# Optimization experiments

Hardware: AMD Instinct MI355X
Metric: run time of the kernel (lower is better)

## Reference

```python
import jax, jax.numpy as jnp
import numpy as np

B, T, N, F_IN = 8, 288, 2000, 1
E, ID, H, K = 128, 16, 128, 20
FL = T // 2 + 1  # rfft length = in_len//2 + 1
EPS_NORM = 1e-12
EPS_LN = 1e-8


def setup_inputs() -> dict:
    key = jax.random.key(0)
    k0, k1, k2, k3, k4 = jax.random.split(key, 5)
    return {
        "x": jax.random.normal(k0, (B, T, N, F_IN), jnp.float32),
        "Ex": jax.random.normal(k1, (FL, E), jnp.float32),
        "nodes": jax.random.normal(k2, (N, ID), jnp.float32),
        "Wd": jax.random.normal(k3, (N, E + ID, H), jnp.float32),
        "Wxabs": jax.random.normal(k4, (H, H), jnp.float32),
    }


def reference(x, Ex, nodes, Wd, Wxabs):
    # [B,T,N,F] -> take feature 0 -> [B,N,T]
    xt = jnp.transpose(x[:, :, :, 0], (0, 2, 1))
    xf = jnp.abs(jnp.fft.rfft(xt, axis=-1))  # [B,N,FL]
    # F.normalize p=2 over dim=1 (nodes), then dim=2 (freq): x / max(||x||, eps)
    xf = xf / jnp.clip(jnp.sqrt(jnp.sum(xf * xf, axis=1, keepdims=True)), EPS_NORM)
    xf = xf / jnp.clip(jnp.sqrt(jnp.sum(xf * xf, axis=2, keepdims=True)), EPS_NORM)
    xe = jnp.matmul(xf, Ex)  # [B,N,E]
    # cat(): append static node identity embedding per batch element
    xk = jnp.concatenate(
        [xe, jnp.broadcast_to(nodes, (xe.shape[0], N, ID))], axis=-1
    )  # [B,N,E+ID]
    # per-node weight bmm: [N,B,E+ID] @ [N,E+ID,H] -> [B,N,H]
    x1 = jax.nn.relu(jnp.einsum('bnd,ndh->bnh', xk, Wd))
    # LayerNorm over last two dims [N,H], eps=1e-8, no affine
    mu = jnp.mean(x1, axis=(1, 2), keepdims=True)
    var = jnp.mean((x1 - mu) ** 2, axis=(1, 2), keepdims=True)
    x2 = (x1 - mu) / jnp.sqrt(var + EPS_LN)
    # dropout is identity at inference
    adp = jnp.einsum('bnh,hk->bnk', x2, Wxabs)  # convt
    adj = jnp.einsum('bnh,bmh->bnm', adp, x1)  # [B,N,N]
    adp = jax.nn.relu(adj)
    # dy_mask_graph: per-row topk over dim=2 (torch dim=1 of the [N,N] slice),
    # binary mask via scatter of ones, then elementwise mask
    _, idx = jax.lax.top_k(adp, K)  # [B,N,K]
    bi = jnp.arange(adp.shape[0])[:, None, None]
    ni = jnp.arange(N)[None, :, None]
    mask = jnp.zeros_like(adp).at[bi, ni, idx].set(1.0)
    adj_masked = adp * mask
    return jax.nn.softmax(adj_masked, axis=2)
```

## Files before the change

kernel.cpp:

```cpp
#include <hip/hip_runtime.h>
#include <math.h>

#define BB 8
#define TT 288
#define NN 2000
#define FLEN 145
#define EE 128
#define IDD 16
#define HH 128
#define DKK 144
#define KTOP 20

#define OFF_TW  ((size_t)0)
#define SZ_TW   ((size_t)TT*FLEN*2)
#define OFF_XF  (OFF_TW + SZ_TW)
#define SZ_XF   ((size_t)BB*FLEN*NN)
#define OFF_ICN (OFF_XF + SZ_XF)
#define OFF_IRN (OFF_ICN + (size_t)BB*FLEN)
#define OFF_XE  (OFF_IRN + (size_t)BB*NN)
#define SZ_BNH  ((size_t)BB*NN*HH)
#define OFF_X1  (OFF_XE + SZ_BNH)
#define OFF_ADP (OFF_X1 + SZ_BNH)
#define OFF_CSW (OFF_ADP + SZ_BNH)
#define OFF_LNS (OFF_CSW + HH)
#define OFF_LNF (OFF_LNS + 16)

__device__ __forceinline__ float wredSum(float v) {
#pragma unroll
  for (int o = 32; o > 0; o >>= 1) v += __shfl_down(v, o, 64);
  return v;
}
__device__ __forceinline__ float wredMax(float v) {
#pragma unroll
  for (int o = 32; o > 0; o >>= 1) v = fmaxf(v, __shfl_down(v, o, 64));
  return v;
}

__global__ void k_init(const float* __restrict__ Wx, float* __restrict__ csw,
                       float* __restrict__ lns) {
  int k = threadIdx.x;
  float s = 0.f;
  for (int h = 0; h < HH; ++h) s += Wx[h * HH + k];
  csw[k] = s;
  if (k < 16) lns[k] = 0.f;
}

__global__ void k_tw(float* __restrict__ tw) {
  int id = blockIdx.x * 256 + threadIdx.x;
  if (id >= TT * FLEN) return;
  int t = id / FLEN, f = id % FLEN;
  int r = (t * f) % TT;
  double th = -2.0 * 3.14159265358979323846 * (double)r / (double)TT;
  tw[2 * id]     = (float)cos(th);
  tw[2 * id + 1] = (float)sin(th);
}

__global__ void k_dft(const float* __restrict__ x, const float* __restrict__ tw,
                      float* __restrict__ xf) {
  __shared__ __align__(16) float Xs[16][128];
  __shared__ __align__(16) float TWs[16][32][2];
  const int b = blockIdx.z;
  const int f0 = blockIdx.y * 32;
  const int n0 = blockIdx.x * 128;
  const int tid = threadIdx.x;
  const int tn = tid & 31;
  const int tf = tid >> 5;
  float ar[4][4] = {}, ai[4][4] = {};
  for (int t0 = 0; t0 < TT; t0 += 16) {
    __syncthreads();
    for (int l = tid; l < 512; l += 256) {
      int row = l >> 5, q = l & 31;
      int n = n0 + q * 4;
      const float* src = x + ((size_t)b * TT + (t0 + row)) * NN + n;
      float4 v = make_float4(0, 0, 0, 0);
      if (n + 3 < NN) v = *(const float4*)src;
      else {
        if (n + 0 < NN) v.x = src[0];
        if (n + 1 < NN) v.y = src[1];
        if (n + 2 < NN) v.z = src[2];
        if (n + 3 < NN) v.w = src[3];
      }
      *(float4*)&Xs[row][q * 4] = v;
    }
    for (int l = tid; l < 512; l += 256) {
      int row = l >> 5, ff = l & 31;
      int f = f0 + ff;
      float2 cs = make_float2(0, 0);
      if (f < FLEN) cs = *(const float2*)&tw[((size_t)(t0 + row) * FLEN + f) * 2];
      *(float2*)&TWs[row][ff][0] = cs;
    }
    __syncthreads();
#pragma unroll 4
    for (int t = 0; t < 16; ++t) {
      float4 xv = *(float4*)&Xs[t][tn * 4];
      float xx[4] = {xv.x, xv.y, xv.z, xv.w};
      float4 p0 = *(float4*)&TWs[t][tf * 4][0];
      float4 p1 = *(float4*)&TWs[t][tf * 4 + 2][0];
      float c[4] = {p0.x, p0.z, p1.x, p1.z};
      float s[4] = {p0.y, p0.w, p1.y, p1.w};
#pragma unroll
      for (int i = 0; i < 4; ++i)
#pragma unroll
        for (int j = 0; j < 4; ++j) {
          ar[i][j] = fmaf(xx[j], c[i], ar[i][j]);
          ai[i][j] = fmaf(xx[j], s[i], ai[i][j]);
        }
    }
  }
#pragma unroll
  for (int i = 0; i < 4; ++i) {
    int f = f0 + tf * 4 + i;
    if (f >= FLEN) continue;
    float* dst = &xf[((size_t)b * FLEN + f) * NN];
    float o[4];
#pragma unroll
    for (int j = 0; j < 4; ++j)
      o[j] = sqrtf(ar[i][j] * ar[i][j] + ai[i][j] * ai[i][j]);
    int n = n0 + tn * 4;
    if (n + 3 < NN) *(float4*)&dst[n] = make_float4(o[0], o[1], o[2], o[3]);
    else {
#pragma unroll
      for (int j = 0; j < 4; ++j) if (n + j < NN) dst[n + j] = o[j];
    }
  }
}

__global__ void k_colnorm(const float* __restrict__ xf, float* __restrict__ icn) {
  __shared__ float sc[4];
  int bf = blockIdx.x;
  const float* rowp = xf + (size_t)bf * NN;
  float s = 0.f;
  for (int i = threadIdx.x; i < NN; i += 256) { float v = rowp[i]; s = fmaf(v, v, s); }
  s = wredSum(s);
  int lane = threadIdx.x & 63, w = threadIdx.x >> 6;
  if (lane == 0) sc[w] = s;
  __syncthreads();
  if (threadIdx.x == 0)
    icn[bf] = 1.f / fmaxf(sqrtf(sc[0] + sc[1] + sc[2] + sc[3]), 1e-12f);
}

__global__ void k_rownorm(const float* __restrict__ xf, const float* __restrict__ icn,
                          float* __restrict__ irn) {
  int b = blockIdx.y;
  int n = blockIdx.x * 256 + threadIdx.x;
  if (n >= NN) return;
  float s = 0.f;
  for (int f = 0; f < FLEN; ++f) {
    float v = xf[((size_t)b * FLEN + f) * NN + n] * icn[b * FLEN + f];
    s = fmaf(v, v, s);
  }
  irn[b * NN + n] = 1.f / fmaxf(sqrtf(s), 1e-12f);
}

__global__ void k_xe(const float* __restrict__ xf, const float* __restrict__ icn,
                     const float* __restrict__ irn, const float* __restrict__ Ex,
                     float* __restrict__ xe) {
  __shared__ __align__(16) float As[16][64];
  __shared__ __align__(16) float Bs[16][128];
  const int b = blockIdx.y;
  const int n0 = blockIdx.x * 64;
  const int tid = threadIdx.x;
  const int tn = tid >> 4, te = tid & 15;
  float acc[4][8] = {};
  for (int f0 = 0; f0 < 160; f0 += 16) {
    __syncthreads();
    {
      int kt = tid >> 4, q = tid & 15;
      int f = f0 + kt;
      int n = n0 + q * 4;
      float4 v = make_float4(0, 0, 0, 0);
      if (f < FLEN) {
        float ic = icn[b * FLEN + f];
        const float* src = &xf[((size_t)b * FLEN + f) * NN + n];
        if (n + 3 < NN) v = *(const float4*)src;
        else {
          if (n + 0 < NN) v.x = src[0];
          if (n + 1 < NN) v.y = src[1];
          if (n + 2 < NN) v.z = src[2];
          if (n + 3 < NN) v.w = src[3];
        }
        v.x *= ic; v.y *= ic; v.z *= ic; v.w *= ic;
      }
      *(float4*)&As[kt][q * 4] = v;
    }
    for (int l = tid; l < 512; l += 256) {
      int kt = l >> 5, q = l & 31;
      int f = f0 + kt;
      float4 v = make_float4(0, 0, 0, 0);
      if (f < FLEN) v = *(const float4*)&Ex[(size_t)f * EE + q * 4];
      *(float4*)&Bs[kt][q * 4] = v;
    }
    __syncthreads();
#pragma unroll
    for (int k = 0; k < 16; ++k) {
      float4 a  = *(float4*)&As[k][tn * 4];
      float4 b0 = *(float4*)&Bs[k][te * 4];
      float4 b1 = *(float4*)&Bs[k][64 + te * 4];
      float av[4] = {a.x, a.y, a.z, a.w};
      float bv[8] = {b0.x, b0.y, b0.z, b0.w, b1.x, b1.y, b1.z, b1.w};
#pragma unroll
      for (int i = 0; i < 4; ++i)
#pragma unroll
        for (int j = 0; j < 8; ++j)
          acc[i][j] = fmaf(av[i], bv[j], acc[i][j]);
    }
  }
#pragma unroll
  for (int i = 0; i < 4; ++i) {
    int n = n0 + tn * 4 + i;
    if (n >= NN) continue;
    float sc = irn[b * NN + n];
    float* dst = &xe[((size_t)b * NN + n) * EE];
    *(float4*)&dst[te * 4] =
        make_float4(acc[i][0] * sc, acc[i][1] * sc, acc[i][2] * sc, acc[i][3] * sc);
    *(float4*)&dst[64 + te * 4] =
        make_float4(acc[i][4] * sc, acc[i][5] * sc, acc[i][6] * sc, acc[i][7] * sc);
  }
}

__global__ void k_x1(const float* __restrict__ xe, const float* __restrict__ nodes,
                     const float* __restrict__ Wd, float* __restrict__ x1) {
  __shared__ __align__(16) float xk[8][DKK];
  const int n = blockIdx.x;
  const int tid = threadIdx.x;
  {
    int b = tid >> 5, q = tid & 31;
    *(float4*)&xk[b][q * 4] = *(const float4*)&xe[((size_t)b * NN + n) * EE + q * 4];
  }
  if (tid < 128) {
    int b = tid >> 4, i = tid & 15;
    xk[b][EE + i] = nodes[(size_t)n * IDD + i];
  }
  __syncthreads();
  const int h = tid & 127;
  const int bg = tid >> 7;
  float acc[4] = {0.f, 0.f, 0.f, 0.f};
  const float* w = Wd + (size_t)n * DKK * HH + h;
  for (int d = 0; d < DKK; ++d) {
    float wv = w[(size_t)d * HH];
#pragma unroll
    for (int j = 0; j < 4; ++j) acc[j] = fmaf(xk[bg + 2 * j][d], wv, acc[j]);
  }
#pragma unroll
  for (int j = 0; j < 4; ++j) {
    int b = bg + 2 * j;
    x1[((size_t)b * NN + n) * HH + h] = fmaxf(acc[j], 0.f);
  }
}

__global__ void k_ln_stats(const float* __restrict__ x1, float* __restrict__ lns) {
  __shared__ float sc[4], sc2[4];
  int b = blockIdx.y, chunk = blockIdx.x;
  const float* base = x1 + (size_t)b * NN * HH + (size_t)chunk * 8000;
  float s = 0.f, s2 = 0.f;
  for (int i = threadIdx.x; i < 8000; i += 256) {
    float v = base[i];
    s += v; s2 = fmaf(v, v, s2);
  }
  s = wredSum(s); s2 = wredSum(s2);
  int lane = threadIdx.x & 63, w = threadIdx.x >> 6;
  if (lane == 0) { sc[w] = s; sc2[w] = s2; }
  __syncthreads();
  if (threadIdx.x == 0) {
    atomicAdd(&lns[b], sc[0] + sc[1] + sc[2] + sc[3]);
    atomicAdd(&lns[8 + b], sc2[0] + sc2[1] + sc2[2] + sc2[3]);
  }
}

__global__ void k_ln_final(const float* __restrict__ lns, float* __restrict__ lnf) {
  int b = threadIdx.x;
  if (b < 8) {
    float cnt = (float)(NN * HH);
    float mu = lns[b] / cnt;
    float var = fmaxf(lns[8 + b] / cnt - mu * mu, 0.f);
    lnf[b] = mu;
    lnf[8 + b] = 1.f / sqrtf(var + 1e-8f);
  }
}

__global__ void k_adp(const float* __restrict__ x1, const float* __restrict__ Wx,
                      const float* __restrict__ csw, const float* __restrict__ lnf,
                      float* __restrict__ adp) {
  __shared__ __align__(16) float As[16][64];
  __shared__ __align__(16) float Bs[16][128];
  const int r0 = blockIdx.x * 64;
  const int tid = threadIdx.x;
  const int tn = tid >> 4, te = tid & 15;
  float acc[4][8] = {};
  for (int k0 = 0; k0 < HH; k0 += 16) {
    __syncthreads();
    {
      int rr = tid >> 2, kq = tid & 3;
      float4 v = *(const float4*)&x1[(size_t)(r0 + rr) * HH + k0 + kq * 4];
      As[kq * 4 + 0][rr] = v.x;
      As[kq * 4 + 1][rr] = v.y;
      As[kq * 4 + 2][rr] = v.z;
      As[kq * 4 + 3][rr] = v.w;
    }
    for (int l = tid; l < 512; l += 256) {
      int kt = l >> 5, q = l & 31;
      *(float4*)&Bs[kt][q * 4] = *(const float4*)&Wx[(size_t)(k0 + kt) * HH + q * 4];
    }
    __syncthreads();
#pragma unroll
    for (int k = 0; k < 16; ++k) {
      float4 a  = *(float4*)&As[k][tn * 4];
      float4 b0 = *(float4*)&Bs[k][te * 4];
      float4 b1 = *(float4*)&Bs[k][64 + te * 4];
      float av[4] = {a.x, a.y, a.z, a.w};
      float bv[8] = {b0.x, b0.y, b0.z, b0.w, b1.x, b1.y, b1.z, b1.w};
#pragma unroll
      for (int i = 0; i < 4; ++i)
#pragma unroll
        for (int j = 0; j < 8; ++j)
          acc[i][j] = fmaf(av[i], bv[j], acc[i][j]);
    }
  }
  float4 c0 = *(const float4*)&csw[te * 4];
  float4 c1 = *(const float4*)&csw[64 + te * 4];
  float cw[8] = {c0.x, c0.y, c0.z, c0.w, c1.x, c1.y, c1.z, c1.w};
#pragma unroll
  for (int i = 0; i < 4; ++i) {
    int r = r0 + tn * 4 + i;
    int b = r / NN;
    float mu = lnf[b], isd = lnf[8 + b];
    float* dst = &adp[(size_t)r * HH];
    float o[8];
#pragma unroll
    for (int j = 0; j < 8; ++j) o[j] = (acc[i][j] - mu * cw[j]) * isd;
    *(float4*)&dst[te * 4] = make_float4(o[0], o[1], o[2], o[3]);
    *(float4*)&dst[64 + te * 4] = make_float4(o[4], o[5], o[6], o[7]);
  }
}

__global__ void k_adj(const float* __restrict__ adp, const float* __restrict__ x1,
                      float* __restrict__ out) {
  __shared__ __align__(16) float As[32][128];
  __shared__ __align__(16) float Bs[32][128];
  const int b = blockIdx.z;
  const int n0 = blockIdx.y * 128;
  const int m0 = blockIdx.x * 128;
  const int tid = threadIdx.x;
  const int tn = tid >> 4, tm = tid & 15;
  float acc[8][8] = {};
  for (int k0 = 0; k0 < HH; k0 += 32) {
    __syncthreads();
    for (int l = tid; l < 1024; l += 256) {
      int row = l >> 3, kq = l & 7;
      int n = n0 + row;
      float4 v = make_float4(0, 0, 0, 0);
      if (n < NN) v = *(const float4*)&adp[((size_t)b * NN + n) * HH + k0 + kq * 4];
      As[kq * 4 + 0][row] = v.x; As[kq * 4 + 1][row] = v.y;
      As[kq * 4 + 2][row] = v.z; As[kq * 4 + 3][row] = v.w;
    }
    for (int l = tid; l < 1024; l += 256) {
      int row = l >> 3, kq = l & 7;
      int m = m0 + row;
      float4 v = make_float4(0, 0, 0, 0);
      if (m < NN) v = *(const float4*)&x1[((size_t)b * NN + m) * HH + k0 + kq * 4];
      Bs[kq * 4 + 0][row] = v.x; Bs[kq * 4 + 1][row] = v.y;
      Bs[kq * 4 + 2][row] = v.z; Bs[kq * 4 + 3][row] = v.w;
    }
    __syncthreads();
#pragma unroll 4
    for (int k = 0; k < 32; ++k) {
      float4 a0 = *(float4*)&As[k][tn * 4];
      float4 a1 = *(float4*)&As[k][64 + tn * 4];
      float4 bq0 = *(float4*)&Bs[k][tm * 4];
      float4 bq1 = *(float4*)&Bs[k][64 + tm * 4];
      float av[8] = {a0.x, a0.y, a0.z, a0.w, a1.x, a1.y, a1.z, a1.w};
      float bv[8] = {bq0.x, bq0.y, bq0.z, bq0.w, bq1.x, bq1.y, bq1.z, bq1.w};
#pragma unroll
      for (int i = 0; i < 8; ++i)
#pragma unroll
        for (int j = 0; j < 8; ++j)
          acc[i][j] = fmaf(av[i], bv[j], acc[i][j]);
    }
  }
  const bool mfull = (m0 + 128 <= NN);
#pragma unroll
  for (int ih = 0; ih < 2; ++ih) {
#pragma unroll
    for (int i = 0; i < 4; ++i) {
      int n = n0 + ih * 64 + tn * 4 + i;
      if (n >= NN) continue;
      float* dst = &out[((size_t)b * NN + n) * NN + m0];
      float r[8];
#pragma unroll
      for (int j = 0; j < 8; ++j) r[j] = fmaxf(acc[ih * 4 + i][j], 0.f);
      if (mfull) {
        *(float4*)&dst[tm * 4] = make_float4(r[0], r[1], r[2], r[3]);
        *(float4*)&dst[64 + tm * 4] = make_float4(r[4], r[5], r[6], r[7]);
      } else {
#pragma unroll
        for (int j = 0; j < 4; ++j) { int m = tm * 4 + j; if (m0 + m < NN) dst[m] = r[j]; }
#pragma unroll
        for (int j = 0; j < 4; ++j) { int m = 64 + tm * 4 + j; if (m0 + m < NN) dst[m] = r[4 + j]; }
      }
    }
  }
}

__global__ void k_softmax(float* __restrict__ out) {
  __shared__ __align__(16) float row[NN];
  __shared__ float scr[4];
  __shared__ float swv[4];
  __shared__ int swi[4];
  __shared__ float tkv[KTOP];
  __shared__ int tki[KTOP];
  __shared__ float bcast[1];
  const int r = blockIdx.x;
  float* g = out + (size_t)r * NN;
  const int tid = threadIdx.x;
  const int lane = tid & 63, w = tid >> 6;
  for (int q = tid; q < 500; q += 256) *(float4*)&row[q * 4] = *(const float4*)&g[q * 4];
  __syncthreads();
  float m = 0.f;
  for (int i = tid; i < NN; i += 256) m = fmaxf(m, row[i]);
  m = wredMax(m);
  if (lane == 0) scr[w] = m;
  __syncthreads();
  m = fmaxf(fmaxf(scr[0], scr[1]), fmaxf(scr[2], scr[3]));
  const float thr = m - 87.f;
  float s = 0.f, c = 0.f;
  for (int i = tid; i < NN; i += 256) {
    float v = row[i];
    if (v > thr) { s += expf(v - m); c += 1.f; }
  }
  s = wredSum(s); c = wredSum(c);
  __syncthreads();
  if (lane == 0) scr[w] = s;
  __syncthreads();
  s = scr[0] + scr[1] + scr[2] + scr[3];
  __syncthreads();
  if (lane == 0) scr[w] = c;
  __syncthreads();
  c = scr[0] + scr[1] + scr[2] + scr[3];
  const float em = expf(-m);
  if (c <= 20.5f) {
    float D = s + ((float)NN - c) * em;
    float invD = 1.f / D;
    float defv = em * invD;
    for (int q = tid; q < 500; q += 256) {
      float4 v = *(float4*)&row[q * 4];
      float4 o;
      o.x = (v.x > thr) ? expf(v.x - m) * invD : defv;
      o.y = (v.y > thr) ? expf(v.y - m) * invD : defv;
      o.z = (v.z > thr) ? expf(v.z - m) * invD : defv;
      o.w = (v.w > thr) ? expf(v.w - m) * invD : defv;
      *(float4*)&g[q * 4] = o;
    }
  } else {
    for (int it = 0; it < KTOP; ++it) {
      float bv = -1.f; int bi = 0x7fffffff;
      for (int i = tid; i < NN; i += 256) {
        float v = row[i];
        if (v > bv) { bv = v; bi = i; }
      }
#pragma unroll
      for (int o = 32; o > 0; o >>= 1) {
        float ov = __shfl_down(bv, o, 64);
        int oi = __shfl_down(bi, o, 64);
        if (ov > bv || (ov == bv && oi < bi)) { bv = ov; bi = oi; }
      }
      __syncthreads();
      if (lane == 0) { swv[w] = bv; swi[w] = bi; }
      __syncthreads();
      if (tid == 0) {
        float fv = swv[0]; int fi = swi[0];
        for (int ww = 1; ww < 4; ++ww)
          if (swv[ww] > fv || (swv[ww] == fv && swi[ww] < fi)) { fv = swv[ww]; fi = swi[ww]; }
        tkv[it] = fv; tki[it] = fi;
        row[fi] = -1.f;
      }
      __syncthreads();
    }
    if (tid == 0) {
      float D = ((float)(NN - KTOP)) * em;
      for (int it = 0; it < KTOP; ++it) D += expf(tkv[it] - m);
      bcast[0] = 1.f / D;
    }
    __syncthreads();
    float invD = bcast[0];
    float defv = em * invD;
    for (int q = tid; q < 500; q += 256)
      *(float4*)&g[q * 4] = make_float4(defv, defv, defv, defv);
    __syncthreads();
    if (tid < KTOP) g[tki[tid]] = expf(tkv[tid] - m) * invD;
  }
}

extern "C" void kernel_launch(void* const* d_in, const int* in_sizes, int n_in,
                              void* d_out, int out_size, void* d_ws, size_t ws_size,
                              hipStream_t stream) {
  const float* x     = (const float*)d_in[0];
  const float* Ex    = (const float*)d_in[1];
  const float* nodes = (const float*)d_in[2];
  const float* Wd    = (const float*)d_in[3];
  const float* Wx    = (const float*)d_in[4];
  float* out = (float*)d_out;
  float* w = (float*)d_ws;
  float* tw  = w + OFF_TW;
  float* xf  = w + OFF_XF;
  float* icn = w + OFF_ICN;
  float* irn = w + OFF_IRN;
  float* xe  = w + OFF_XE;
  float* x1  = w + OFF_X1;
  float* adp = w + OFF_ADP;
  float* csw = w + OFF_CSW;
  float* lns = w + OFF_LNS;
  float* lnf = w + OFF_LNF;

  k_init<<<1, 128, 0, stream>>>(Wx, csw, lns);
  k_tw<<<(TT * FLEN + 255) / 256, 256, 0, stream>>>(tw);
  k_dft<<<dim3(16, 5, BB), 256, 0, stream>>>(x, tw, xf);
  k_colnorm<<<BB * FLEN, 256, 0, stream>>>(xf, icn);
  k_rownorm<<<dim3(8, BB), 256, 0, stream>>>(xf, icn, irn);
  k_xe<<<dim3(32, BB), 256, 0, stream>>>(xf, icn, irn, Ex, xe);
  k_x1<<<NN, 256, 0, stream>>>(xe, nodes, Wd, x1);
  k_ln_stats<<<dim3(32, BB), 256, 0, stream>>>(x1, lns);
  k_ln_final<<<1, 64, 0, stream>>>(lns, lnf);
  k_adp<<<250, 256, 0, stream>>>(x1, Wx, csw, lnf, adp);
  k_adj<<<dim3(16, 16, BB), 256, 0, stream>>>(adp, x1, out);
  k_softmax<<<BB * NN, 256, 0, stream>>>(out);
}
```

Before: 541.0 us.

## Use split-fp16 MFMA for adjacency GEMM and restructure per-node x1 matmul

```diff
diff --git a/kernel.cpp b/kernel.cpp
--- a/kernel.cpp
+++ b/kernel.cpp
@@ -10,6 +10,10 @@
 #define HH 128
 #define DKK 144
 #define KTOP 20
+
+typedef _Float16 half8 __attribute__((ext_vector_type(8)));
+typedef float f32x4 __attribute__((ext_vector_type(4)));
+typedef unsigned short ushort_t;
 
 #define OFF_TW  ((size_t)0)
 #define SZ_TW   ((size_t)TT*FLEN*2)
@@ -34,6 +38,14 @@
 #pragma unroll
   for (int o = 32; o > 0; o >>= 1) v = fmaxf(v, __shfl_down(v, o, 64));
   return v;
+}
+
+__device__ __forceinline__ void split16(float v, ushort_t& hi, ushort_t& lo) {
+  _Float16 h = (_Float16)v;
+  _Float16 l = (_Float16)(v - (float)h);
+  union { _Float16 f; ushort_t u; } a, b;
+  a.f = h; b.f = l;
+  hi = a.u; lo = b.u;
 }
 
 __global__ void k_init(const float* __restrict__ Wx, float* __restrict__ csw,
@@ -218,9 +230,11 @@
   }
 }
 
-__global__ void k_x1(const float* __restrict__ xe, const float* __restrict__ nodes,
-                     const float* __restrict__ Wd, float* __restrict__ x1) {
+__global__ void k_x1(const float* xe, const float* __restrict__ nodes,
+                     const float* __restrict__ Wd, float* __restrict__ x1,
+                     ushort_t* x1hl) {
   __shared__ __align__(16) float xk[8][DKK];
+  __shared__ float red[4][32][33];
   const int n = blockIdx.x;
   const int tid = threadIdx.x;
   {
@@ -232,19 +246,47 @@
     xk[b][EE + i] = nodes[(size_t)n * IDD + i];
   }
   __syncthreads();
-  const int h = tid & 127;
-  const int bg = tid >> 7;
-  float acc[4] = {0.f, 0.f, 0.f, 0.f};
-  const float* w = Wd + (size_t)n * DKK * HH + h;
-  for (int d = 0; d < DKK; ++d) {
-    float wv = w[(size_t)d * HH];
-#pragma unroll
-    for (int j = 0; j < 4; ++j) acc[j] = fmaf(xk[bg + 2 * j][d], wv, acc[j]);
-  }
-#pragma unroll
-  for (int j = 0; j < 4; ++j) {
-    int b = bg + 2 * j;
-    x1[((size_t)b * NN + n) * HH + h] = fmaxf(acc[j], 0.f);
+  const int h4 = tid & 31;
+  const int dg = tid >> 5;
+  float acc[8][4] = {};
+  for (int d = dg; d < DKK; d += 8) {
+    float4 wv = *(const float4*)&Wd[((size_t)n * DKK + d) * HH + h4 * 4];
+#pragma unroll
+    for (int b = 0; b < 8; ++b) {
+      float xv = xk[b][d];
+      acc[b][0] = fmaf(xv, wv.x, acc[b][0]);
+      acc[b][1] = fmaf(xv, wv.y, acc[b][1]);
+      acc[b][2] = fmaf(xv, wv.z, acc[b][2]);
+      acc[b][3] = fmaf(xv, wv.w, acc[b][3]);
+    }
+  }
+#pragma unroll
+  for (int b = 0; b < 8; ++b)
+#pragma unroll
+    for (int j = 0; j < 4; ++j)
+      acc[b][j] += __shfl_xor(acc[b][j], 32, 64);
+  const int wv_ = tid >> 6, lane = tid & 63;
+  if (lane < 32) {
+#pragma unroll
+    for (int b = 0; b < 8; ++b)
+#pragma unroll
+      for (int j = 0; j < 4; ++j)
+        red[wv_][lane][b * 4 + j] = acc[b][j];
+  }
+  __syncthreads();
+#pragma unroll
+  for (int o = 0; o < 4; ++o) {
+    int idx = tid + o * 256;
+    int b = idx >> 7, h = idx & 127;
+    float s = red[0][h >> 2][b * 4 + (h & 3)] + red[1][h >> 2][b * 4 + (h & 3)] +
+              red[2][h >> 2][b * 4 + (h & 3)] + red[3][h >> 2][b * 4 + (h & 3)];
+    s = fmaxf(s, 0.f);
+    x1[((size_t)b * NN + n) * HH + h] = s;
+    ushort_t hi, lo;
+    split16(s, hi, lo);
+    size_t base = ((size_t)b * NN + n) * 256;
+    x1hl[base + h] = hi;
+    x1hl[base + 128 + h] = lo;
   }
 }
 
@@ -280,7 +322,7 @@
 
 __global__ void k_adp(const float* __restrict__ x1, const float* __restrict__ Wx,
                       const float* __restrict__ csw, const float* __restrict__ lnf,
-                      float* __restrict__ adp) {
+                      ushort_t* __restrict__ adphl) {
   __shared__ __align__(16) float As[16][64];
   __shared__ __align__(16) float Bs[16][128];
   const int r0 = blockIdx.x * 64;
@@ -324,78 +366,97 @@
     int r = r0 + tn * 4 + i;
     int b = r / NN;
     float mu = lnf[b], isd = lnf[8 + b];
-    float* dst = &adp[(size_t)r * HH];
-    float o[8];
-#pragma unroll
-    for (int j = 0; j < 8; ++j) o[j] = (acc[i][j] - mu * cw[j]) * isd;
-    *(float4*)&dst[te * 4] = make_float4(o[0], o[1], o[2], o[3]);
-    *(float4*)&dst[64 + te * 4] = make_float4(o[4], o[5], o[6], o[7]);
-  }
-}
-
-__global__ void k_adj(const float* __restrict__ adp, const float* __restrict__ x1,
+    size_t base = (size_t)r * 256;
+    ushort_t hi[8], lo[8];
+#pragma unroll
+    for (int j = 0; j < 8; ++j) {
+      float o = (acc[i][j] - mu * cw[j]) * isd;
+      split16(o, hi[j], lo[j]);
+    }
+    ushort4 u;
+    u.x = hi[0]; u.y = hi[1]; u.z = hi[2]; u.w = hi[3];
+    *(ushort4*)&adphl[base + te * 4] = u;
+    u.x = hi[4]; u.y = hi[5]; u.z = hi[6]; u.w = hi[7];
+    *(ushort4*)&adphl[base + 64 + te * 4] = u;
+    u.x = lo[0]; u.y = lo[1]; u.z = lo[2]; u.w = lo[3];
+    *(ushort4*)&adphl[base + 128 + te * 4] = u;
+    u.x = lo[4]; u.y = lo[5]; u.z = lo[6]; u.w = lo[7];
+    *(ushort4*)&adphl[base + 128 + 64 + te * 4] = u;
+  }
+}
+
+__global__ void k_adj(const ushort_t* __restrict__ adphl,
+                      const ushort_t* __restrict__ x1hl,
                       float* __restrict__ out) {
-  __shared__ __align__(16) float As[32][128];
-  __shared__ __align__(16) float Bs[32][128];
+  __shared__ __align__(16) ushort_t lds[4][128 * 32];
   const int b = blockIdx.z;
   const int n0 = blockIdx.y * 128;
   const int m0 = blockIdx.x * 128;
   const int tid = threadIdx.x;
-  const int tn = tid >> 4, tm = tid & 15;
-  float acc[8][8] = {};
+  const int w = tid >> 6;
+  const int lane = tid & 63;
+  const int quad = lane >> 4, r16 = lane & 15;
+  const int rBase = (w >> 1) * 64;
+  const int cBase = (w & 1) * 64;
+
+  f32x4 acc[4][4];
+#pragma unroll
+  for (int i = 0; i < 4; ++i)
+#pragma unroll
+    for (int j = 0; j < 4; ++j)
+      acc[i][j] = (f32x4){0.f, 0.f, 0.f, 0.f};
+
+  const ushort_t* src = (w < 2) ? adphl : x1hl;
+  const int rg0 = (w < 2) ? n0 : m0;
+  const int loOff = (w & 1) ? 128 : 0;
+
   for (int k0 = 0; k0 < HH; k0 += 32) {
     __syncthreads();
-    for (int l = tid; l < 1024; l += 256) {
-      int row = l >> 3, kq = l & 7;
-      int n = n0 + row;
-      float4 v = make_float4(0, 0, 0, 0);
-      if (n < NN) v = *(const float4*)&adp[((size_t)b * NN + n) * HH + k0 + kq * 4];
-      As[kq * 4 + 0][row] = v.x; As[kq * 4 + 1][row] = v.y;
-      As[kq * 4 + 2][row] = v.z; As[kq * 4 + 3][row] = v.w;
-    }
-    for (int l = tid; l < 1024; l += 256) {
-      int row = l >> 3, kq = l & 7;
-      int m = m0 + row;
-      float4 v = make_float4(0, 0, 0, 0);
-      if (m < NN) v = *(const float4*)&x1[((size_t)b * NN + m) * HH + k0 + kq * 4];
-      Bs[kq * 4 + 0][row] = v.x; Bs[kq * 4 + 1][row] = v.y;
-      Bs[kq * 4 + 2][row] = v.z; Bs[kq * 4 + 3][row] = v.w;
-    }
-    __syncthreads();
-#pragma unroll 4
-    for (int k = 0; k < 32; ++k) {
-      float4 a0 = *(float4*)&As[k][tn * 4];
-      float4 a1 = *(float4*)&As[k][64 + tn * 4];
-      float4 bq0 = *(float4*)&Bs[k][tm * 4];
-      float4 bq1 = *(float4*)&Bs[k][64 + tm * 4];
-      float av[8] = {a0.x, a0.y, a0.z, a0.w, a1.x, a1.y, a1.z, a1.w};
-      float bv[8] = {bq0.x, bq0.y, bq0.z, bq0.w, bq1.x, bq1.y, bq1.z, bq1.w};
-#pragma unroll
-      for (int i = 0; i < 8; ++i)
-#pragma unroll
-        for (int j = 0; j < 8; ++j)
-          acc[i][j] = fmaf(av[i], bv[j], acc[i][j]);
-    }
-  }
-  const bool mfull = (m0 + 128 <= NN);
-#pragma unroll
-  for (int ih = 0; ih < 2; ++ih) {
+#pragma unroll
+    for (int i = 0; i < 8; ++i) {
+      int cl = i * 64 + lane;
+      int row = cl >> 2, c = cl & 3;
+      int gr = rg0 + row; if (gr > NN - 1) gr = NN - 1;
+      const uint4* gp =
+          (const uint4*)(src + ((size_t)(b * NN + gr)) * 256 + loOff + k0 + c * 8);
+      uint4 v = *gp;
+      *(uint4*)&lds[w][row * 32 + ((c ^ (row & 3)) * 8)] = v;
+    }
+    __syncthreads();
+
+    half8 Ah[4], Al[4], Bh[4], Bl[4];
 #pragma unroll
     for (int i = 0; i < 4; ++i) {
-      int n = n0 + ih * 64 + tn * 4 + i;
-      if (n >= NN) continue;
-      float* dst = &out[((size_t)b * NN + n) * NN + m0];
-      float r[8];
-#pragma unroll
-      for (int j = 0; j < 8; ++j) r[j] = fmaxf(acc[ih * 4 + i][j], 0.f);
-      if (mfull) {
-        *(float4*)&dst[tm * 4] = make_float4(r[0], r[1], r[2], r[3]);
-        *(float4*)&dst[64 + tm * 4] = make_float4(r[4], r[5], r[6], r[7]);
-      } else {
-#pragma unroll
-        for (int j = 0; j < 4; ++j) { int m = tm * 4 + j; if (m0 + m < NN) dst[m] = r[j]; }
-#pragma unroll
-        for (int j = 0; j < 4; ++j) { int m = 64 + tm * 4 + j; if (m0 + m < NN) dst[m] = r[4 + j]; }
+      int ar = rBase + i * 16 + r16;
+      int aoff = ar * 32 + ((quad ^ (ar & 3)) * 8);
+      Ah[i] = *(half8*)&lds[0][aoff];
+      Al[i] = *(half8*)&lds[1][aoff];
+      int br = cBase + i * 16 + r16;
+      int boff = br * 32 + ((quad ^ (br & 3)) * 8);
+      Bh[i] = *(half8*)&lds[2][boff];
+      Bl[i] = *(half8*)&lds[3][boff];
+    }
+#pragma unroll
+    for (int i = 0; i < 4; ++i)
+#pragma unroll
+      for (int j = 0; j < 4; ++j) {
+        acc[i][j] = __builtin_amdgcn_mfma_f32_16x16x32_f16(Ah[i], Bh[j], acc[i][j], 0, 0, 0);
+        acc[i][j] = __builtin_amdgcn_mfma_f32_16x16x32_f16(Ah[i], Bl[j], acc[i][j], 0, 0, 0);
+        acc[i][j] = __builtin_amdgcn_mfma_f32_16x16x32_f16(Al[i], Bh[j], acc[i][j], 0, 0, 0);
+      }
+  }
+
+#pragma unroll
+  for (int i = 0; i < 4; ++i) {
+#pragma unroll
+    for (int j = 0; j < 4; ++j) {
+      int m = m0 + cBase + j * 16 + r16;
+      if (m >= NN) continue;
+#pragma unroll
+      for (int reg = 0; reg < 4; ++reg) {
+        int n = n0 + rBase + i * 16 + quad * 4 + reg;
+        if (n >= NN) continue;
+        out[((size_t)b * NN + n) * NN + m] = fmaxf(acc[i][j][reg], 0.f);
       }
     }
   }
@@ -506,10 +567,11 @@
   float* irn = w + OFF_IRN;
   float* xe  = w + OFF_XE;
   float* x1  = w + OFF_X1;
-  float* adp = w + OFF_ADP;
   float* csw = w + OFF_CSW;
   float* lns = w + OFF_LNS;
   float* lnf = w + OFF_LNF;
+  ushort_t* adphl = (ushort_t*)(w + OFF_ADP);
+  ushort_t* x1hl  = (ushort_t*)(w + OFF_XE);
 
   k_init<<<1, 128, 0, stream>>>(Wx, csw, lns);
   k_tw<<<(TT * FLEN + 255) / 256, 256, 0, stream>>>(tw);
@@ -517,10 +579,10 @@
   k_colnorm<<<BB * FLEN, 256, 0, stream>>>(xf, icn);
   k_rownorm<<<dim3(8, BB), 256, 0, stream>>>(xf, icn, irn);
   k_xe<<<dim3(32, BB), 256, 0, stream>>>(xf, icn, irn, Ex, xe);
-  k_x1<<<NN, 256, 0, stream>>>(xe, nodes, Wd, x1);
+  k_x1<<<NN, 256, 0, stream>>>(xe, nodes, Wd, x1, x1hl);
   k_ln_stats<<<dim3(32, BB), 256, 0, stream>>>(x1, lns);
   k_ln_final<<<1, 64, 0, stream>>>(lns, lnf);
-  k_adp<<<250, 256, 0, stream>>>(x1, Wx, csw, lnf, adp);
-  k_adj<<<dim3(16, 16, BB), 256, 0, stream>>>(adp, x1, out);
+  k_adp<<<250, 256, 0, stream>>>(x1, Wx, csw, lnf, adphl);
+  k_adj<<<dim3(16, 16, BB), 256, 0, stream>>>(adphl, x1hl, out);
   k_softmax<<<BB * NN, 256, 0, stream>>>(out);
 }
```

Result: faster. 488.2 us (-9.8%).
